# Optimization experiments

Measured on AMD Instinct MI355X. Metric: run time of the kernel, lower is better.

Reference implementation:

```python
import jax, jax.numpy as jnp
import numpy as np

B, H, W, D = 8, 56, 56, 256
NH = 8
KD = D // NH  # 32, key_dim == head_dim (value_factor=1)
FFN = 1024
EPS = 1e-6
SCALE = KD ** -0.5


def _lin(x, w, b):
    # torch nn.Linear: y = x @ W^T + b, W is (out, in)
    return jnp.einsum('...i,oi->...o', x, w) + b


def _ln(x, g, b):
    mu = jnp.mean(x, axis=-1, keepdims=True)
    var = jnp.mean(jnp.square(x - mu), axis=-1, keepdims=True)
    return (x - mu) * jax.lax.rsqrt(var + EPS) * g + b


def _dwconv(x, kernel, bias):
    # x: (B,H,W,C) NHWC, kernel: (kh,kw,1,C) HWIO depthwise
    y = jax.lax.conv_general_dilated(
        x, kernel, window_strides=(1, 1), padding='SAME',
        dimension_numbers=('NHWC', 'HWIO', 'NHWC'),
        feature_group_count=x.shape[-1])
    return y + bias


def _rope_sincos(h, w, head_dim):
    # PosEncodingGen: angle freq repeated pairwise, index over flattened H*W
    angle = 1.0 / (10000.0 ** jnp.linspace(0.0, 1.0, head_dim // 2))
    angle = jnp.repeat(angle, 2)  # (head_dim,)
    idx = jnp.arange(h * w, dtype=jnp.float32)
    phase = idx[:, None] * angle[None, :]
    return jnp.sin(phase).reshape(h, w, head_dim), jnp.cos(phase).reshape(h, w, head_dim)


def _angle_transform(x, sin, cos):
    # x: (B,NH,H,W,KD); sin/cos: (H,W,KD) broadcast over (B,NH)
    x1 = x[..., ::2]
    x2 = x[..., 1::2]
    rot = jnp.stack([-x2, x1], axis=-1).reshape(x.shape)
    return x * cos + rot * sin


def setup_inputs() -> dict:
    key = jax.random.key(0)
    ks = jax.random.split(key, 16)
    s = 0.02
    return {
        'x': jax.random.normal(ks[0], (B, H, W, D), jnp.float32),
        'cpe_w': jax.random.normal(ks[1], (3, 3, 1, D), jnp.float32) * s,
        'cpe_b': jnp.zeros((D,), jnp.float32),
        'ln1_g': jnp.ones((D,), jnp.float32),
        'ln1_b': jnp.zeros((D,), jnp.float32),
        'wq': jax.random.normal(ks[2], (D, D), jnp.float32) * s,
        'bq': jnp.zeros((D,), jnp.float32),
        'wk': jax.random.normal(ks[3], (D, D), jnp.float32) * s,
        'bk': jnp.zeros((D,), jnp.float32),
        'wv': jax.random.normal(ks[4], (D, D), jnp.float32) * s,
        'bv': jnp.zeros((D,), jnp.float32),
        'lepe_w': jax.random.normal(ks[5], (5, 5, 1, D), jnp.float32) * s,
        'lepe_b': jnp.zeros((D,), jnp.float32),
        'wo': jax.random.normal(ks[6], (D, D), jnp.float32) * s,
        'bo': jnp.zeros((D,), jnp.float32),
        'ln2_g': jnp.ones((D,), jnp.float32),
        'ln2_b': jnp.zeros((D,), jnp.float32),
        'fc1_w': jax.random.normal(ks[7], (FFN, D), jnp.float32) * s,
        'fc1_b': jnp.zeros((FFN,), jnp.float32),
        'dw_w': jax.random.normal(ks[8], (3, 3, 1, FFN), jnp.float32) * s,
        'dw_b': jnp.zeros((FFN,), jnp.float32),
        'fc2_w': jax.random.normal(ks[9], (D, FFN), jnp.float32) * s,
        'fc2_b': jnp.zeros((D,), jnp.float32),
    }


def _decomposed_gsa(x, sin, cos, wq, bq, wk, bk, wv, bv, lepe_w, lepe_b, wo, bo):
    b, h, w, d = x.shape
    q = _lin(x, wq, bq)
    k = _lin(x, wk, bk) * SCALE
    v = _lin(x, wv, bv)
    lepe = _dwconv(v, lepe_w, lepe_b)  # (b,h,w,d)
    # -> (b, nh, h, w, kd)
    q = q.reshape(b, h, w, NH, KD).transpose(0, 3, 1, 2, 4)
    k = k.reshape(b, h, w, NH, KD).transpose(0, 3, 1, 2, 4)
    v = v.reshape(b, h, w, NH, KD).transpose(0, 3, 1, 2, 4)
    qr = _angle_transform(q, sin, cos)
    kr = _angle_transform(k, sin, cos)
    # attention along W axis (per row h)
    aw = jnp.einsum('bnhik,bnhjk->bnhij', qr, kr)  # (b,nh,h,w,w)
    aw = jax.nn.softmax(aw, axis=-1)
    vw = jnp.einsum('bnhij,bnhjd->bnhid', aw, v)   # (b,nh,h,w,kd)
    # attention along H axis (per column w)
    ah = jnp.einsum('bniwk,bnjwk->bnwij', qr, kr)  # (b,nh,w,h,h)
    ah = jax.nn.softmax(ah, axis=-1)
    out = jnp.einsum('bnwij,bnjwd->bniwd', ah, vw)  # (b,nh,h,w,kd)
    # faithful to torch: flat reinterpret of (b,nh,h,w,kd) -> (b,h,w,nh*kd)
    out = out.reshape(b, h, w, NH * KD)
    out = out + lepe
    return _lin(out, wo, bo)


def reference(x, cpe_w, cpe_b, ln1_g, ln1_b, wq, bq, wk, bk, wv, bv,
              lepe_w, lepe_b, wo, bo, ln2_g, ln2_b,
              fc1_w, fc1_b, dw_w, dw_b, fc2_w, fc2_b):
    b, h, w, d = x.shape
    x = x + _dwconv(x, cpe_w, cpe_b)
    sin, cos = _rope_sincos(h, w, KD)
    # attention sub-block
    shortcut = x
    xn = _ln(x, ln1_g, ln1_b)
    attn = _decomposed_gsa(xn, sin, cos, wq, bq, wk, bk, wv, bv,
                           lepe_w, lepe_b, wo, bo)
    x = shortcut + attn  # drop_path=Identity, gamma_1=1.0
    # FFN sub-block (subconv=True, subln=False)
    shortcut = x
    xn = _ln(x, ln2_g, ln2_b)
    hdn = jax.nn.gelu(_lin(xn, fc1_w, fc1_b), approximate=False)
    hdn = _dwconv(hdn, dw_w, dw_b) + hdn
    ffn_out = _lin(hdn, fc2_w, fc2_b)
    return shortcut + ffn_out
```

## Files before the change

### kernel.cpp

```cpp
#include <hip/hip_runtime.h>
#include <hip/hip_bf16.h>
#include <math.h>

typedef __hip_bfloat16 bf16;

#define HB 8
#define HH 56
#define WWD 56
#define DD 256
#define NHEAD 8
#define KDIM 32
#define FFND 1024
#define NPIX (HB*HH*WWD)
#define SCALE_K 0.17677669529663687f

typedef __attribute__((ext_vector_type(8))) short short8;
typedef __attribute__((ext_vector_type(4))) float f32x4;

__device__ inline float toF(float x){ return x; }
__device__ inline float toF(bf16 x){ return __bfloat162float(x); }

__device__ inline float bfu_to_f(unsigned short u){
    union { float f; unsigned u32; } cv; cv.u32 = (unsigned)u << 16; return cv.f;
}

__device__ inline unsigned short f2bu(float f){
    union { bf16 b; unsigned short u; } cv; cv.b = __float2bfloat16(f); return cv.u;
}
__device__ inline unsigned pk2(float a, float b){
    return (unsigned)f2bu(a) | ((unsigned)f2bu(b) << 16);
}

__device__ inline float gelu_fast(float y){
    const float u2 = y*y;
    const float arg = y * (2.302208219f + 0.1029402445f*u2);
    const float e2 = exp2f(fminf(arg, 126.0f));
    return y * e2 / (e2 + 1.0f);
}

__device__ inline void gl16(const bf16* g, unsigned short* l){
    __builtin_amdgcn_global_load_lds((const __attribute__((address_space(1))) void*)g,
                                     (__attribute__((address_space(3))) void*)l, 16, 0, 0);
}

__global__ __launch_bounds__(256) void wcvt_kernel(
    const float* __restrict__ wq, const float* __restrict__ wk,
    const float* __restrict__ wv, const float* __restrict__ wo,
    const float* __restrict__ f1, const float* __restrict__ f2,
    bf16* __restrict__ dst)
{
    const int id = blockIdx.x*256 + threadIdx.x;
    const float* src; int off;
    if      (id < 8192)  { src = wq; off = id; }
    else if (id < 16384) { src = wk; off = id - 8192; }
    else if (id < 24576) { src = wv; off = id - 16384; }
    else if (id < 32768) { src = wo; off = id - 24576; }
    else if (id < 65536) { src = f1; off = id - 32768; }
    else                 { src = f2; off = id - 65536; }
    const float4 a = *(const float4*)(src + (size_t)off*8);
    const float4 b = *(const float4*)(src + (size_t)off*8 + 4);
    uint4 v; v.x = pk2(a.x,a.y); v.y = pk2(a.z,a.w); v.z = pk2(b.x,b.y); v.w = pk2(b.z,b.w);
    *(uint4*)(dst + (size_t)id*8) = v;
}

__global__ __launch_bounds__(256) void rope_init_kernel(float2* __restrict__ t)
{
    const int id = blockIdx.x*256 + threadIdx.x;
    const int idx = id >> 4, i = id & 15;
    const float ph = (float)idx * exp2f(-(float)i * 0.88584749196996324f);
    t[id] = make_float2(cosf(ph), sinf(ph));
}

__global__ __launch_bounds__(256) void cpe_ln_slide_kernel(
    const float* __restrict__ x, const float* __restrict__ wt,
    const float* __restrict__ bias, const float* __restrict__ g,
    const float* __restrict__ bln, float* __restrict__ X0, bf16* __restrict__ B1)
{
    constexpr int C = 256, VEC = 4, NPX = 4, KS = 3, P = 1, NX = NPX + KS - 1;
    constexpr int GPR = WWD / NPX;
    constexpr int NB  = NPIX / (NPX * 4);
    const int tid  = threadIdx.x;
    const int wv   = tid >> 6;
    const int lane = tid & 63;
    const int bid  = blockIdx.x;
    const int swb  = (bid & 7) * (NB >> 3) + (bid >> 3);
    const int gid  = swb * 4 + wv;
    const int row  = gid / GPR;
    const int w0   = (gid % GPR) * NPX;
    const int h    = row % HH;
    const int b    = row / HH;
    const int c0   = lane * VEC;

    float acc[NPX][VEC];
    {
        const float4 b0 = *(const float4*)(bias + c0);
        #pragma unroll
        for (int j = 0; j < NPX; j++) {
            acc[j][0] = b0.x; acc[j][1] = b0.y; acc[j][2] = b0.z; acc[j][3] = b0.w;
        }
    }

    #pragma unroll
    for (int ky = 0; ky < KS; ky++) {
        const int hh = h + ky - P;
        if (hh < 0 || hh >= HH) continue;
        const float* rowp = x + ((size_t)(b*HH + hh) * WWD) * C + c0;
        float wvv[KS][VEC];
        #pragma unroll
        for (int kx = 0; kx < KS; kx++) {
            const float4 w4 = *(const float4*)(wt + (size_t)(ky*KS + kx)*C + c0);
            wvv[kx][0] = w4.x; wvv[kx][1] = w4.y; wvv[kx][2] = w4.z; wvv[kx][3] = w4.w;
        }
        #pragma unroll
        for (int xc = 0; xc < NX; xc++) {
            const int ww = w0 - P + xc;
            float4 f0 = {0.f, 0.f, 0.f, 0.f};
            if (ww >= 0 && ww < WWD) f0 = *(const float4*)(rowp + (size_t)ww*C);
            const float fv[VEC] = {f0.x, f0.y, f0.z, f0.w};
            #pragma unroll
            for (int j = 0; j < NPX; j++) {
                const int kx = xc - j;
                if (kx < 0 || kx >= KS) continue;
                #pragma unroll
                for (int e = 0; e < VEC; e++)
                    acc[j][e] += fv[e] * wvv[kx][e];
            }
        }
    }

    const float4 gv = *(const float4*)(g + c0);
    const float4 bv = *(const float4*)(bln + c0);
    #pragma unroll
    for (int j = 0; j < NPX; j++) {
        const size_t obase = ((size_t)row*WWD + w0 + j)*C + c0;
        {
            const float4 r0 = *(const float4*)(x + obase);
            acc[j][0] += r0.x; acc[j][1] += r0.y; acc[j][2] += r0.z; acc[j][3] += r0.w;
        }
        { float4 o; o.x = acc[j][0]; o.y = acc[j][1]; o.z = acc[j][2]; o.w = acc[j][3];
          *(float4*)(X0 + obase) = o; }
        float s1 = acc[j][0] + acc[j][1] + acc[j][2] + acc[j][3];
        float s2 = acc[j][0]*acc[j][0] + acc[j][1]*acc[j][1]
                 + acc[j][2]*acc[j][2] + acc[j][3]*acc[j][3];
        #pragma unroll
        for (int d = 1; d < 64; d <<= 1) { s1 += __shfl_xor(s1, d); s2 += __shfl_xor(s2, d); }
        const float mu  = s1 * (1.0f/DD);
        const float var = s2 * (1.0f/DD) - mu*mu;
        const float inv = rsqrtf(var + 1e-6f);
        uint2 o2;
        o2.x = pk2((acc[j][0]-mu)*inv*gv.x + bv.x, (acc[j][1]-mu)*inv*gv.y + bv.y);
        o2.y = pk2((acc[j][2]-mu)*inv*gv.z + bv.z, (acc[j][3]-mu)*inv*gv.w + bv.w);
        *(uint2*)(B1 + obase) = o2;
    }
}

template<int KS, bool ADD, int C>
__global__ __launch_bounds__(256) void dwconv_slide_kernel(
    const bf16* __restrict__ in, const float* __restrict__ wt, int wst,
    const float* __restrict__ bias, bf16* __restrict__ out)
{
    constexpr int VEC = 8, CG = C/VEC, GPB = 256/CG, NPX = 4, P = KS/2, NX = NPX+KS-1;
    constexpr int GPR = WWD/NPX;
    constexpr int NB  = NPIX/(NPX*GPB);
    const int tid = threadIdx.x;
    const int cg  = tid % CG;
    const int gl  = tid / CG;
    const int bid = blockIdx.x;
    const int swb = (bid & 7) * (NB >> 3) + (bid >> 3);
    const int gid = swb * GPB + gl;
    const int row = gid / GPR;
    const int w0  = (gid % GPR) * NPX;
    const int h   = row % HH;
    const int b   = row / HH;
    const int c0  = cg * VEC;

    float acc[NPX][VEC];
    {
        const float4 b0 = *(const float4*)(bias + c0);
        const float4 b1 = *(const float4*)(bias + c0 + 4);
        #pragma unroll
        for (int j = 0; j < NPX; j++) {
            acc[j][0]=b0.x; acc[j][1]=b0.y; acc[j][2]=b0.z; acc[j][3]=b0.w;
            acc[j][4]=b1.x; acc[j][5]=b1.y; acc[j][6]=b1.z; acc[j][7]=b1.w;
        }
    }

    #pragma unroll
    for (int ky = 0; ky < KS; ky++) {
        const int hh = h + ky - P;
        if (hh < 0 || hh >= HH) continue;
        const bf16* rowp = in + ((size_t)(b*HH + hh) * WWD) * C + c0;
        float wv[KS][VEC];
        #pragma unroll
        for (int kx = 0; kx < KS; kx++) {
            const float* wp = wt + (size_t)(ky*KS + kx)*wst + c0;
            const float4 w0v = *(const float4*)(wp);
            const float4 w1v = *(const float4*)(wp + 4);
            wv[kx][0]=w0v.x; wv[kx][1]=w0v.y; wv[kx][2]=w0v.z; wv[kx][3]=w0v.w;
            wv[kx][4]=w1v.x; wv[kx][5]=w1v.y; wv[kx][6]=w1v.z; wv[kx][7]=w1v.w;
        }
        #pragma unroll
        for (int x = 0; x < NX; x++) {
            const int ww = w0 - P + x;
            short8 raw = {0,0,0,0,0,0,0,0};
            if (ww >= 0 && ww < WWD) raw = *(const short8*)(rowp + (size_t)ww*C);
            float f[VEC];
            #pragma unroll
            for (int e = 0; e < VEC; e++) f[e] = bfu_to_f((unsigned short)raw[e]);
            #pragma unroll
            for (int j = 0; j < NPX; j++) {
                const int kx = x - j;
                if (kx < 0 || kx >= KS) continue;
                #pragma unroll
                for (int e = 0; e < VEC; e++)
                    acc[j][e] += f[e] * wv[kx][e];
            }
        }
    }

    #pragma unroll
    for (int j = 0; j < NPX; j++) {
        const size_t obase = ((size_t)row*WWD + w0 + j)*C + c0;
        if constexpr (ADD) {
            short8 vv = *(const short8*)(in + obase);
            #pragma unroll
            for (int e = 0; e < VEC; e++) acc[j][e] += bfu_to_f((unsigned short)vv[e]);
        }
        uint4 o;
        o.x = pk2(acc[j][0], acc[j][1]); o.y = pk2(acc[j][2], acc[j][3]);
        o.z = pk2(acc[j][4], acc[j][5]); o.w = pk2(acc[j][6], acc[j][7]);
        *(uint4*)(out + obase) = o;
    }
}

template<int EPI, int ROPE>
__global__ __launch_bounds__(256) void mgemm128_kernel(
    const bf16* __restrict__ A, const bf16* __restrict__ Wb, int ldw,
    const float* __restrict__ bias, const float2* __restrict__ ropet,
    const float* __restrict__ residF, float* __restrict__ accF,
    bf16* __restrict__ outB, bf16* __restrict__ outK, bf16* __restrict__ outV,
    int M, int N, int K, float scale)
{
    __shared__ __align__(16) unsigned short Sh[24576];
    const int tid  = threadIdx.x;
    const int wid  = tid >> 6;
    const int lane = tid & 63;
    const int quad = lane >> 4;
    const int l15  = lane & 15;
    const int wr   = wid >> 1;
    const int wc   = wid & 1;

    const int NXg = gridDim.x;
    const int T   = NXg * gridDim.y;
    int f = blockIdx.y * NXg + blockIdx.x;
    f = (f & 7) * (T >> 3) + (f >> 3);
    const int row0 = (f / NXg) * 128;
    const int col0 = (f % NXg) * 128;

    f32x4 acc[4][4];
    #pragma unroll
    for (int m = 0; m < 4; m++)
        #pragma unroll
        for (int n = 0; n < 4; n++)
            acc[m][n] = (f32x4){0.f, 0.f, 0.f, 0.f};

    const int ob0 = (wid*2 + 0)*64;
    const int ob1 = (wid*2 + 1)*64;
    const int o0  = ob0 + lane, o1 = ob1 + lane;
    const int rA0 = o0 >> 2, ch0 = (o0 & 3)*8;
    const int rA1 = o1 >> 2, ch1 = (o1 & 3)*8;
    const bf16* pA0 = A  + (size_t)(row0 + rA0)*K   + ch0;
    const bf16* pA1 = A  + (size_t)(row0 + rA1)*K   + ch1;
    const bf16* pW0 = Wb + (size_t)(col0 + rA0)*ldw + ch0;
    const bf16* pW1 = Wb + (size_t)(col0 + rA1)*ldw + ch1;

    #define STAGE(bi) { unsigned short* As_ = Sh + (bi)*8192;                  \
                        unsigned short* Bs_ = As_ + 4096;                      \
                        gl16(pA0, &As_[ob0*8]); gl16(pA1, &As_[ob1*8]);        \
                        gl16(pW0, &Bs_[ob0*8]); gl16(pW1, &Bs_[ob1*8]);        \
                        pA0 += 32; pA1 += 32; pW0 += 32; pW1 += 32; }

    #define COMPUTE(bi) { const unsigned short* As_ = Sh + (bi)*8192;          \
                          const unsigned short* Bs_ = As_ + 4096;              \
                          short8 af[4], bfr[4];                                \
                          _Pragma("unroll")                                    \
                          for (int m = 0; m < 4; m++)                          \
                              af[m] = *(const short8*)(&As_[(wr*64 + m*16 + l15)*32 + quad*8]); \
                          _Pragma("unroll")                                    \
                          for (int n = 0; n < 4; n++)                          \
                              bfr[n] = *(const short8*)(&Bs_[(wc*64 + n*16 + l15)*32 + quad*8]); \
                          _Pragma("unroll")                                    \
                          for (int m = 0; m < 4; m++)                          \
                              _Pragma("unroll")                                \
                              for (int n = 0; n < 4; n++)                      \
                                  acc[m][n] = __builtin_amdgcn_mfma_f32_16x16x32_bf16(af[m], bfr[n], acc[m][n], 0, 0, 0); }

    const int nt = K >> 5;
    STAGE(0); STAGE(1);
    int cur = 0;
    for (int t = 0; t < nt; t++) {
        if (t + 2 < nt) {
            const int nx = (cur == 0) ? 2 : ((cur == 1) ? 0 : 1);
            STAGE(nx);
            asm volatile("s_waitcnt vmcnt(8)" ::: "memory");
        } else if (t + 1 < nt) {
            asm volatile("s_waitcnt vmcnt(4)" ::: "memory");
        } else {
            asm volatile("s_waitcnt vmcnt(0)" ::: "memory");
        }
        __builtin_amdgcn_s_barrier();
        COMPUTE(cur);
        if (t + 1 < nt) __builtin_amdgcn_s_barrier();
        cur = (cur == 2) ? 0 : cur + 1;
    }
    #undef STAGE
    #undef COMPUTE

    __syncthreads();
    float* Ls = (float*)Sh;
    const int cbl = l15 * 4;
    const int seg = (EPI == 3) ? (col0 >> 8) : 0;
    bf16* dst = outB;
    if (EPI == 3) dst = (seg == 0) ? outB : ((seg == 1) ? outK : outV);
    const float esc = (EPI == 3) ? ((seg == 1) ? scale : 1.0f) : scale;
    const bool doRope = ROPE && (EPI != 3 || seg < 2);

    #pragma unroll
    for (int m = 0; m < 4; m++) {
        #pragma unroll
        for (int n = 0; n < 4; n++) {
            const int col = n*16 + l15;
            const float bval = bias[col0 + wc*64 + col];
            #pragma unroll
            for (int reg = 0; reg < 4; reg++) {
                float y = (acc[m][n][reg] + bval) * esc;
                if (EPI == 1) y = gelu_fast(y);
                Ls[wid*1088 + (quad*4+reg)*68 + col] = y;
            }
        }
        #pragma unroll
        for (int p = 0; p < 4; p++) {
            const int rowt = p*4 + quad;
            const float4 v = *(const float4*)&Ls[wid*1088 + rowt*68 + cbl];
            const int mm = row0 + wr*64 + m*16 + rowt;
            if (EPI == 2) {
                const size_t o = (size_t)mm * N + col0 + wc*64 + cbl;
                const float4 rv = *(const float4*)(residF + o);
                float4 w; w.x = v.x+rv.x; w.y = v.y+rv.y; w.z = v.z+rv.z; w.w = v.w+rv.w;
                *(float4*)(accF + o) = w;
            } else {
                const int ncl = (EPI == 3) ? ((col0 & 255) + wc*64 + cbl)
                                           : (col0 + wc*64 + cbl);
                const size_t o = (EPI == 3) ? ((size_t)mm * 256 + ncl)
                                            : ((size_t)mm * N + ncl);
                float a = v.x, b = v.y, c = v.z, d = v.w;
                if (doRope) {
                    const int idx = mm % (HH*WWD);
                    const int i0 = (ncl & 31) >> 1;
                    const float4 t = *(const float4*)&ropet[(size_t)idx*16 + i0];
                    const float na  = a*t.x - b*t.y;
                    const float nb  = b*t.x + a*t.y;
                    const float ncv = c*t.z - d*t.w;
                    const float nd  = d*t.z + c*t.w;
                    a = na; b = nb; c = ncv; d = nd;
                }
                uint2 ov; ov.x = pk2(a, b); ov.y = pk2(c, d);
                *(uint2*)(dst + o) = ov;
            }
        }
        if (m < 3) __syncthreads();
    }
}

__global__ __launch_bounds__(512) void mgemm_wo_ln_kernel(
    const bf16* __restrict__ A, const bf16* __restrict__ Wb,
    const float* __restrict__ bias, const float* __restrict__ residF,
    float* __restrict__ accF, const float* __restrict__ g,
    const float* __restrict__ bln, bf16* __restrict__ outB)
{
    __shared__ __align__(16) unsigned short Sh[24576];
    const int tid  = threadIdx.x;
    const int wid  = tid >> 6;
    const int lane = tid & 63;
    const int quad = lane >> 4;
    const int l15  = lane & 15;
    const int wr   = wid >> 2;
    const int wc   = wid & 3;
    const int row0 = blockIdx.x * 128;

    f32x4 acc[4][4];
    #pragma unroll
    for (int m = 0; m < 4; m++)
        #pragma unroll
        for (int n = 0; n < 4; n++)
            acc[m][n] = (f32x4){0.f, 0.f, 0.f, 0.f};

    const int rU = wid*16 + (lane >> 2);
    const int ch = (lane & 3) * 8;
    const bf16* pA  = A  + (size_t)(row0 + rU)*256 + ch;
    const bf16* pB1 = Wb + (size_t)rU*256 + ch;
    const bf16* pB2 = Wb + (size_t)(128 + rU)*256 + ch;

    #define STAGE(bi) { unsigned short* As_ = Sh + (bi)*12288;                 \
                        unsigned short* Bs_ = As_ + 4096;                      \
                        gl16(pA,  &As_[wid*512]);                              \
                        gl16(pB1, &Bs_[wid*512]);                              \
                        gl16(pB2, &Bs_[4096 + wid*512]);                       \
                        pA += 32; pB1 += 32; pB2 += 32; }

    #define COMPUTE(bi) { const unsigned short* As_ = Sh + (bi)*12288;         \
                          const unsigned short* Bs_ = As_ + 4096;              \
                          short8 af[4], bfr[4];                                \
                          _Pragma("unroll")                                    \
                          for (int m = 0; m < 4; m++)                          \
                              af[m] = *(const short8*)(&As_[(wr*64 + m*16 + l15)*32 + quad*8]); \
                          _Pragma("unroll")                                    \
                          for (int n = 0; n < 4; n++)                          \
                              bfr[n] = *(const short8*)(&Bs_[(wc*64 + n*16 + l15)*32 + quad*8]); \
                          _Pragma("unroll")                                    \
                          for (int m = 0; m < 4; m++)                          \
                              _Pragma("unroll")                                \
                              for (int n = 0; n < 4; n++)                      \
                                  acc[m][n] = __builtin_amdgcn_mfma_f32_16x16x32_bf16(af[m], bfr[n], acc[m][n], 0, 0, 0); }

    STAGE(0);
    int cur = 0;
    for (int t = 0; t < 8; t++) {
        if (t < 7) {
            STAGE(cur ^ 1);
            asm volatile("s_waitcnt vmcnt(3)" ::: "memory");
        } else {
            asm volatile("s_waitcnt vmcnt(0)" ::: "memory");
        }
        __builtin_amdgcn_s_barrier();
        COMPUTE(cur);
        if (t < 7) __builtin_amdgcn_s_barrier();
        cur ^= 1;
    }
    #undef STAGE
    #undef COMPUTE

    __syncthreads();
    float* Ls = (float*)Sh;
    float* SL = Ls + 8*1088;
    const int cbl = l15 * 4;
    float4 stash[4][4];

    #pragma unroll
    for (int m = 0; m < 4; m++) {
        #pragma unroll
        for (int n = 0; n < 4; n++) {
            const float bval = bias[wc*64 + n*16 + l15];
            const int col = n*16 + l15;
            #pragma unroll
            for (int reg = 0; reg < 4; reg++)
                Ls[wid*1088 + (quad*4+reg)*68 + col] = acc[m][n][reg] + bval;
        }
        #pragma unroll
        for (int p = 0; p < 4; p++) {
            const int rowt = p*4 + quad;
            const float4 v = *(const float4*)&Ls[wid*1088 + rowt*68 + cbl];
            const int rl = wr*64 + m*16 + rowt;
            const size_t o = (size_t)(row0 + rl) * 256 + wc*64 + cbl;
            const float4 rv = *(const float4*)(residF + o);
            float4 w; w.x = v.x+rv.x; w.y = v.y+rv.y; w.z = v.z+rv.z; w.w = v.w+rv.w;
            *(float4*)(accF + o) = w;
            stash[m][p] = w;
            float ls1 = w.x + w.y + w.z + w.w;
            float ls2 = w.x*w.x + w.y*w.y + w.z*w.z + w.w*w.w;
            #pragma unroll
            for (int d = 1; d < 16; d <<= 1) {
                ls1 += __shfl_xor(ls1, d);
                ls2 += __shfl_xor(ls2, d);
            }
            if (l15 == 0) { SL[rl*8 + wc*2] = ls1; SL[rl*8 + wc*2 + 1] = ls2; }
        }
    }
    __syncthreads();
    if (tid < 128) {
        const int row = tid;
        const float s1 = SL[row*8] + SL[row*8+2] + SL[row*8+4] + SL[row*8+6];
        const float s2 = SL[row*8+1] + SL[row*8+3] + SL[row*8+5] + SL[row*8+7];
        const float mu  = s1 * (1.0f/256.0f);
        const float var = s2 * (1.0f/256.0f) - mu*mu;
        SL[row*8]   = mu;
        SL[row*8+1] = rsqrtf(var + 1e-6f);
    }
    __syncthreads();
    const float4 g4 = *(const float4*)(g   + wc*64 + cbl);
    const float4 b4 = *(const float4*)(bln + wc*64 + cbl);
    #pragma unroll
    for (int m = 0; m < 4; m++) {
        #pragma unroll
        for (int p = 0; p < 4; p++) {
            const int rl = wr*64 + m*16 + p*4 + quad;
            const float mu  = SL[rl*8];
            const float inv = SL[rl*8+1];
            const float4 w = stash[m][p];
            uint2 ov;
            ov.x = pk2((w.x-mu)*inv*g4.x + b4.x, (w.y-mu)*inv*g4.y + b4.y);
            ov.y = pk2((w.z-mu)*inv*g4.z + b4.z, (w.w-mu)*inv*g4.w + b4.w);
            *(uint2*)(outB + (size_t)(row0 + rl)*256 + wc*64 + cbl) = ov;
        }
    }
}

template<bool COLM>
__global__ __launch_bounds__(256) void attn_mfma_kernel(
    const bf16* __restrict__ q, const bf16* __restrict__ k,
    const bf16* __restrict__ v, const bf16* __restrict__ lepe,
    bf16* __restrict__ outp)
{
    __shared__ unsigned short Qb[64*40];
    __shared__ unsigned short Kb[64*40];
    __shared__ unsigned short Vt[32*80];
    __shared__ unsigned short Pb[64*72];

    const int bid  = blockIdx.x;
    const int line = bid % 56;
    const int nh   = (bid / 56) % NHEAD;
    const int b    = bid / (56 * NHEAD);
    const int tid  = threadIdx.x;
    const int wid  = tid >> 6;
    const int lane = tid & 63;
    const int quad = lane >> 4;
    const int l15  = lane & 15;

    const size_t rstr = COLM ? (size_t)WWD * DD : (size_t)DD;
    const size_t base = COLM ? (((size_t)b*HH*WWD + line) * DD + nh*KDIM)
                             : (((size_t)(b*HH + line) * WWD) * DD + nh*KDIM);

    {
        const int r  = tid >> 2;
        const int cc = tid & 3;
        uint4 zero = {0,0,0,0};
        if (r < 56) {
            size_t gg = base + (size_t)r * rstr + cc*8;
            *(uint4*)(&Qb[r*40 + cc*8]) = *(const uint4*)(q + gg);
            *(uint4*)(&Kb[r*40 + cc*8]) = *(const uint4*)(k + gg);
        } else {
            *(uint4*)(&Qb[r*40 + cc*8]) = zero;
            *(uint4*)(&Kb[r*40 + cc*8]) = zero;
        }
        uint4 vv = zero;
        if (lane < 56)
            vv = *(const uint4*)(v + base + (size_t)lane * rstr + wid*8);
        const unsigned short* pv = (const unsigned short*)&vv;
        #pragma unroll
        for (int e = 0; e < 8; e++)
            Vt[(wid*8 + e)*80 + lane] = pv[e];
    }
    __syncthreads();

    {
        short8 af = *(const short8*)(&Qb[(wid*16 + l15)*40 + quad*8]);
        f32x4 s_[4];
        __builtin_amdgcn_s_setprio(1);
        #pragma unroll
        for (int j = 0; j < 4; j++) {
            short8 bfm = *(const short8*)(&Kb[(j*16 + l15)*40 + quad*8]);
            f32x4 z = {0.f,0.f,0.f,0.f};
            s_[j] = __builtin_amdgcn_mfma_f32_16x16x32_bf16(af, bfm, z, 0, 0, 0);
        }
        __builtin_amdgcn_s_setprio(0);
        const bool v3 = (l15 < 8);
        float mx[4], sm[4];
        #pragma unroll
        for (int reg = 0; reg < 4; reg++) {
            float m01 = fmaxf(s_[0][reg], s_[1][reg]);
            float m23 = v3 ? fmaxf(s_[2][reg], s_[3][reg]) : s_[2][reg];
            mx[reg] = fmaxf(m01, m23);
        }
        #pragma unroll
        for (int d = 1; d < 16; d <<= 1) {
            #pragma unroll
            for (int reg = 0; reg < 4; reg++)
                mx[reg] = fmaxf(mx[reg], __shfl_xor(mx[reg], d));
        }
        float e_[4][4];
        #pragma unroll
        for (int reg = 0; reg < 4; reg++) sm[reg] = 0.f;
        #pragma unroll
        for (int j = 0; j < 4; j++) {
            #pragma unroll
            for (int reg = 0; reg < 4; reg++) {
                const bool valid = (j < 3) || v3;
                float ex = valid ? expf(s_[j][reg] - mx[reg]) : 0.f;
                e_[j][reg] = ex;
                sm[reg] += ex;
            }
        }
        #pragma unroll
        for (int d = 1; d < 16; d <<= 1) {
            #pragma unroll
            for (int reg = 0; reg < 4; reg++)
                sm[reg] += __shfl_xor(sm[reg], d);
        }
        float inv[4];
        #pragma unroll
        for (int reg = 0; reg < 4; reg++) inv[reg] = 1.0f / sm[reg];
        #pragma unroll
        for (int j = 0; j < 4; j++)
            #pragma unroll
            for (int reg = 0; reg < 4; reg++)
                Pb[(wid*16 + quad*4 + reg)*72 + j*16 + l15] = f2bu(e_[j][reg] * inv[reg]);
    }
    __syncthreads();

    {
        f32x4 acc[2];
        acc[0] = (f32x4){0.f,0.f,0.f,0.f};
        acc[1] = (f32x4){0.f,0.f,0.f,0.f};
        __builtin_amdgcn_s_setprio(1);
        #pragma unroll
        for (int k0 = 0; k0 < 64; k0 += 32) {
            short8 af = *(const short8*)(&Pb[(wid*16 + l15)*72 + k0 + quad*8]);
            #pragma unroll
            for (int nt = 0; nt < 2; nt++) {
                short8 bfm = *(const short8*)(&Vt[(nt*16 + l15)*80 + k0 + quad*8]);
                acc[nt] = __builtin_amdgcn_mfma_f32_16x16x32_bf16(af, bfm, acc[nt], 0, 0, 0);
            }
        }
        __builtin_amdgcn_s_setprio(0);
        #pragma unroll
        for (int nt = 0; nt < 2; nt++) {
            #pragma unroll
            for (int reg = 0; reg < 4; reg++) {
                const int m = wid*16 + quad*4 + reg;
                const int d = nt*16 + l15;
                if (m < 56) {
                    float val = acc[nt][reg];
                    if (COLM) {
                        int hp = 7*nh + (m >> 3);
                        int wp = (m & 7)*7 + (line >> 3);
                        int cp = (line & 7)*32 + d;
                        size_t o = ((size_t)(b*HH + hp)*WWD + wp)*DD + cp;
                        outp[o] = __float2bfloat16(val + toF(lepe[o]));
                    } else {
                        outp[base + (size_t)m * rstr + d] = __float2bfloat16(val);
                    }
                }
            }
        }
    }
}

extern "C" void kernel_launch(void* const* d_in, const int* in_sizes, int n_in,
                              void* d_out, int out_size, void* d_ws, size_t ws_size,
                              hipStream_t stream)
{
    const float* x_in   = (const float*)d_in[0];
    const float* cpe_w  = (const float*)d_in[1];
    const float* cpe_b  = (const float*)d_in[2];
    const float* ln1_g  = (const float*)d_in[3];
    const float* ln1_b  = (const float*)d_in[4];
    const float* wq     = (const float*)d_in[5];
    const float* bq     = (const float*)d_in[6];
    const float* wk     = (const float*)d_in[7];
    const float* bk     = (const float*)d_in[8];
    const float* wv     = (const float*)d_in[9];
    const float* bv     = (const float*)d_in[10];
    const float* lepe_w = (const float*)d_in[11];
    const float* lepe_b = (const float*)d_in[12];
    const float* wo     = (const float*)d_in[13];
    const float* bo     = (const float*)d_in[14];
    const float* ln2_g  = (const float*)d_in[15];
    const float* ln2_b  = (const float*)d_in[16];
    const float* fc1_w  = (const float*)d_in[17];
    const float* fc1_b  = (const float*)d_in[18];
    const float* dw_w   = (const float*)d_in[19];
    const float* dw_b   = (const float*)d_in[20];
    const float* fc2_w  = (const float*)d_in[21];
    const float* fc2_b  = (const float*)d_in[22];
    float* out = (float*)d_out;

    const size_t ND = (size_t)NPIX * DD;
    const size_t NF = (size_t)NPIX * FFND;
    char* ws = (char*)d_ws;
    float*  X0    = (float*)(ws);
    float*  ACC   = (float*)(ws + ND*4);
    bf16*   B1    = (bf16*) (ws + ND*8);
    bf16*   B2    = (bf16*) (ws + ND*8 + ND*2);
    bf16*   H1    = (bf16*) (ws + ND*8 + ND*4);
    bf16*   H2    = (bf16*) (ws + ND*8 + ND*4 + NF*2);
    bf16*   WB    = (bf16*) (ws + ND*8 + ND*4 + NF*4);
    float2* ROPET = (float2*)(ws + ND*8 + ND*4 + NF*4 + 786432*2);
    float*  BQKV  = (float*) (ws + ND*8 + ND*4 + NF*4 + 786432*2 + 50176*8);
    bf16*   B3 = H1;
    bf16*   B4 = H2;
    bf16*   VWb   = (bf16*)d_out;
    bf16*   ATTNb = VWb + ND;

    const bf16* WOb = WB + 196608;
    const bf16* F1b = WB + 262144;
    const bf16* F2b = WB + 524288;

    dim3 b256(256);
    dim3 gridQKV(768/128, NPIX/128);
    dim3 gridD(DD/128, NPIX/128);
    dim3 gridF(FFND/128, NPIX/128);

    wcvt_kernel<<<384, b256, 0, stream>>>(wq, wk, wv, wo, fc1_w, fc2_w, WB);
    rope_init_kernel<<<196, b256, 0, stream>>>(ROPET);
    hipMemcpyAsync(BQKV,       bq, 256*sizeof(float), hipMemcpyDeviceToDevice, stream);
    hipMemcpyAsync(BQKV + 256, bk, 256*sizeof(float), hipMemcpyDeviceToDevice, stream);
    hipMemcpyAsync(BQKV + 512, bv, 256*sizeof(float), hipMemcpyDeviceToDevice, stream);
    cpe_ln_slide_kernel<<<NPIX/16, b256, 0, stream>>>(x_in, cpe_w, cpe_b, ln1_g, ln1_b, X0, B1);
    mgemm128_kernel<3,1><<<gridQKV, b256, 0, stream>>>(B1, WB, DD, BQKV, ROPET,
                                                       nullptr, nullptr, B2, B3, B4,
                                                       NPIX, 768, DD, SCALE_K);
    dwconv_slide_kernel<5, false, 256><<<784, b256, 0, stream>>>(B4, lepe_w, DD, lepe_b, B1);
    attn_mfma_kernel<false><<<HB*NHEAD*HH, b256, 0, stream>>>(B2, B3, B4, nullptr, VWb);
    attn_mfma_kernel<true><<<HB*NHEAD*WWD, b256, 0, stream>>>(B2, B3, VWb, B1, ATTNb);
    mgemm_wo_ln_kernel<<<196, dim3(512), 0, stream>>>(ATTNb, WOb, bo, X0, ACC, ln2_g, ln2_b, B2);
    mgemm128_kernel<1,0><<<gridF, b256, 0, stream>>>(B2, F1b, DD, fc1_b, nullptr,
                                                     nullptr, nullptr, H1, nullptr, nullptr,
                                                     NPIX, FFND, DD, 1.0f);
    dwconv_slide_kernel<3, true, 1024><<<3136, b256, 0, stream>>>(H1, dw_w, FFND, dw_b, H2);
    mgemm128_kernel<2,0><<<gridD, b256, 0, stream>>>(H2, F2b, FFND, fc2_b, nullptr,
                                                     ACC, out, nullptr, nullptr, nullptr,
                                                     NPIX, DD, FFND, 1.0f);
}
```

Measured before the change: 326.5 us.

## Swizzle GEMM LDS tiles, merge init kernels, drop epilogue syncthreads

XOR-swizzles the 16-byte chunk index in the LDS tiles of both MFMA GEMM kernels, on the global_load_lds writes and the fragment reads, to cut LDS bank conflicts. Merges the weight conversion, RoPE table init and three bias memcpys into one init kernel to save launch overhead. Also removes a __syncthreads inside the GEMM epilogue loop, which could introduce a race if that epilogue reuses shared memory.

```diff
diff --git a/kernel.cpp b/kernel.cpp
--- a/kernel.cpp
+++ b/kernel.cpp
@@ -43,32 +43,36 @@
                                      (__attribute__((address_space(3))) void*)l, 16, 0, 0);
 }
 
-__global__ __launch_bounds__(256) void wcvt_kernel(
+__global__ __launch_bounds__(256) void init_kernel(
     const float* __restrict__ wq, const float* __restrict__ wk,
     const float* __restrict__ wv, const float* __restrict__ wo,
     const float* __restrict__ f1, const float* __restrict__ f2,
-    bf16* __restrict__ dst)
+    const float* __restrict__ bq, const float* __restrict__ bk,
+    const float* __restrict__ bv,
+    bf16* __restrict__ dst, float2* __restrict__ ropet, float* __restrict__ bqkv)
 {
     const int id = blockIdx.x*256 + threadIdx.x;
-    const float* src; int off;
-    if      (id < 8192)  { src = wq; off = id; }
-    else if (id < 16384) { src = wk; off = id - 8192; }
-    else if (id < 24576) { src = wv; off = id - 16384; }
-    else if (id < 32768) { src = wo; off = id - 24576; }
-    else if (id < 65536) { src = f1; off = id - 32768; }
-    else                 { src = f2; off = id - 65536; }
-    const float4 a = *(const float4*)(src + (size_t)off*8);
-    const float4 b = *(const float4*)(src + (size_t)off*8 + 4);
-    uint4 v; v.x = pk2(a.x,a.y); v.y = pk2(a.z,a.w); v.z = pk2(b.x,b.y); v.w = pk2(b.z,b.w);
-    *(uint4*)(dst + (size_t)id*8) = v;
-}
-
-__global__ __launch_bounds__(256) void rope_init_kernel(float2* __restrict__ t)
-{
-    const int id = blockIdx.x*256 + threadIdx.x;
-    const int idx = id >> 4, i = id & 15;
-    const float ph = (float)idx * exp2f(-(float)i * 0.88584749196996324f);
-    t[id] = make_float2(cosf(ph), sinf(ph));
+    if (id < 98304) {
+        const float* src; int off;
+        if      (id < 8192)  { src = wq; off = id; }
+        else if (id < 16384) { src = wk; off = id - 8192; }
+        else if (id < 24576) { src = wv; off = id - 16384; }
+        else if (id < 32768) { src = wo; off = id - 24576; }
+        else if (id < 65536) { src = f1; off = id - 32768; }
+        else                 { src = f2; off = id - 65536; }
+        const float4 a = *(const float4*)(src + (size_t)off*8);
+        const float4 b = *(const float4*)(src + (size_t)off*8 + 4);
+        uint4 v; v.x = pk2(a.x,a.y); v.y = pk2(a.z,a.w); v.z = pk2(b.x,b.y); v.w = pk2(b.z,b.w);
+        *(uint4*)(dst + (size_t)id*8) = v;
+    } else if (id < 148480) {
+        const int rid = id - 98304;
+        const int idx = rid >> 4, i = rid & 15;
+        const float ph = (float)idx * exp2f(-(float)i * 0.88584749196996324f);
+        ropet[rid] = make_float2(cosf(ph), sinf(ph));
+    } else {
+        const int b = id - 148480;
+        bqkv[b] = (b < 256) ? bq[b] : ((b < 512) ? bk[b-256] : bv[b-512]);
+    }
 }
 
 __global__ __launch_bounds__(256) void cpe_ln_slide_kernel(
@@ -249,6 +253,7 @@
     const int l15  = lane & 15;
     const int wr   = wid >> 1;
     const int wc   = wid & 1;
+    const int sw   = (l15 >> 1) & 3;
 
     const int NXg = gridDim.x;
     const int T   = NXg * gridDim.y;
@@ -267,8 +272,8 @@
     const int ob0 = (wid*2 + 0)*64;
     const int ob1 = (wid*2 + 1)*64;
     const int o0  = ob0 + lane, o1 = ob1 + lane;
-    const int rA0 = o0 >> 2, ch0 = (o0 & 3)*8;
-    const int rA1 = o1 >> 2, ch1 = (o1 & 3)*8;
+    const int rA0 = o0 >> 2, ch0 = ((o0 & 3) ^ ((o0 >> 3) & 3)) * 8;
+    const int rA1 = o1 >> 2, ch1 = ((o1 & 3) ^ ((o1 >> 3) & 3)) * 8;
     const bf16* pA0 = A  + (size_t)(row0 + rA0)*K   + ch0;
     const bf16* pA1 = A  + (size_t)(row0 + rA1)*K   + ch1;
     const bf16* pW0 = Wb + (size_t)(col0 + rA0)*ldw + ch0;
@@ -285,10 +290,10 @@
                           short8 af[4], bfr[4];                                \
                           _Pragma("unroll")                                    \
                           for (int m = 0; m < 4; m++)                          \
-                              af[m] = *(const short8*)(&As_[(wr*64 + m*16 + l15)*32 + quad*8]); \
+                              af[m] = *(const short8*)(&As_[(wr*64 + m*16 + l15)*32 + (quad ^ sw)*8]); \
                           _Pragma("unroll")                                    \
                           for (int n = 0; n < 4; n++)                          \
-                              bfr[n] = *(const short8*)(&Bs_[(wc*64 + n*16 + l15)*32 + quad*8]); \
+                              bfr[n] = *(const short8*)(&Bs_[(wc*64 + n*16 + l15)*32 + (quad ^ sw)*8]); \
                           _Pragma("unroll")                                    \
                           for (int m = 0; m < 4; m++)                          \
                               _Pragma("unroll")                                \
@@ -368,7 +373,6 @@
                 *(uint2*)(dst + o) = ov;
             }
         }
-        if (m < 3) __syncthreads();
     }
 }
 
@@ -386,6 +390,7 @@
     const int l15  = lane & 15;
     const int wr   = wid >> 2;
     const int wc   = wid & 3;
+    const int sw   = (l15 >> 1) & 3;
     const int row0 = blockIdx.x * 128;
 
     f32x4 acc[4][4];
@@ -396,7 +401,7 @@
             acc[m][n] = (f32x4){0.f, 0.f, 0.f, 0.f};
 
     const int rU = wid*16 + (lane >> 2);
-    const int ch = (lane & 3) * 8;
+    const int ch = ((lane & 3) ^ ((lane >> 3) & 3)) * 8;
     const bf16* pA  = A  + (size_t)(row0 + rU)*256 + ch;
     const bf16* pB1 = Wb + (size_t)rU*256 + ch;
     const bf16* pB2 = Wb + (size_t)(128 + rU)*256 + ch;
@@ -413,10 +418,10 @@
                           short8 af[4], bfr[4];                                \
                           _Pragma("unroll")                                    \
                           for (int m = 0; m < 4; m++)                          \
-                              af[m] = *(const short8*)(&As_[(wr*64 + m*16 + l15)*32 + quad*8]); \
+                              af[m] = *(const short8*)(&As_[(wr*64 + m*16 + l15)*32 + (quad ^ sw)*8]); \
                           _Pragma("unroll")                                    \
                           for (int n = 0; n < 4; n++)                          \
-                              bfr[n] = *(const short8*)(&Bs_[(wc*64 + n*16 + l15)*32 + quad*8]); \
+                              bfr[n] = *(const short8*)(&Bs_[(wc*64 + n*16 + l15)*32 + (quad ^ sw)*8]); \
                           _Pragma("unroll")                                    \
                           for (int m = 0; m < 4; m++)                          \
                               _Pragma("unroll")                                \
@@ -700,11 +705,8 @@
     dim3 gridD(DD/128, NPIX/128);
     dim3 gridF(FFND/128, NPIX/128);
 
-    wcvt_kernel<<<384, b256, 0, stream>>>(wq, wk, wv, wo, fc1_w, fc2_w, WB);
-    rope_init_kernel<<<196, b256, 0, stream>>>(ROPET);
-    hipMemcpyAsync(BQKV,       bq, 256*sizeof(float), hipMemcpyDeviceToDevice, stream);
-    hipMemcpyAsync(BQKV + 256, bk, 256*sizeof(float), hipMemcpyDeviceToDevice, stream);
-    hipMemcpyAsync(BQKV + 512, bv, 256*sizeof(float), hipMemcpyDeviceToDevice, stream);
+    init_kernel<<<583, b256, 0, stream>>>(wq, wk, wv, wo, fc1_w, fc2_w,
+                                          bq, bk, bv, WB, ROPET, BQKV);
     cpe_ln_slide_kernel<<<NPIX/16, b256, 0, stream>>>(x_in, cpe_w, cpe_b, ln1_g, ln1_b, X0, B1);
     mgemm128_kernel<3,1><<<gridQKV, b256, 0, stream>>>(B1, WB, DD, BQKV, ROPET,
                                                        nullptr, nullptr, B2, B3, B4,
```

New measurement: 318.9 us. 1.02x faster.
